# Performance work log

Measured on AMD Instinct MI355X. Metric: run time of the kernel, lower is better.

## Reference

```python
import jax, jax.numpy as jnp
import numpy as np

T, H, I, E, TOPK = 4096, 2880, 2880, 16, 4
EPS = 1e-5
ALPHA = 1.702


def setup_inputs() -> dict:
    key = jax.random.key(0)
    ks = jax.random.split(key, 8)
    s = 0.02
    return {
        "x": jax.random.normal(ks[0], (T, H), dtype=jnp.float32),
        "norm_w": jnp.ones((H,), dtype=jnp.float32),
        "gate_w": jax.random.normal(ks[1], (E, H), dtype=jnp.float32) * s,
        "gate_b": jax.random.normal(ks[2], (E,), dtype=jnp.float32) * s,
        "w1": jax.random.normal(ks[3], (E, 2 * I, H), dtype=jnp.float32) * s,  # fused gate_up
        "b1": jax.random.normal(ks[4], (E, 2 * I), dtype=jnp.float32) * s,
        "w2": jax.random.normal(ks[5], (E, H, I), dtype=jnp.float32) * s,      # down proj
        "b2": jax.random.normal(ks[6], (E, H), dtype=jnp.float32) * s,
    }


def _rmsnorm(x, w, eps=EPS):
    var = jnp.mean(x * x, axis=-1, keepdims=True)
    return x * jax.lax.rsqrt(var + eps) * w


def _swiglu(gu):
    glu, lin = jnp.split(gu, 2, axis=-1)
    return glu * jax.nn.sigmoid(ALPHA * glu) * (lin + 1.0)


def reference(x, norm_w, gate_w, gate_b, w1, b1, w2, b2):
    t = _rmsnorm(x, norm_w)                       # [T, H]
    logits = t @ gate_w.T + gate_b                # [T, E]
    # Renormalize routing: top-k of logits, softmax over the k selected logits
    vals, idx = jax.lax.top_k(logits, TOPK)       # [T, k]
    wts = jax.nn.softmax(vals, axis=-1)           # [T, k]
    combine = jnp.zeros((t.shape[0], E), dtype=t.dtype)
    combine = combine.at[jnp.arange(t.shape[0])[:, None], idx].set(wts)  # [T, E]
    out = jnp.zeros_like(x)
    for e in range(E):                            # small fixed expert loop
        gu = t @ w1[e].T + b1[e]                  # [T, 2I]
        y = _swiglu(gu) @ w2[e].T + b2[e]         # [T, H]
        out = out + combine[:, e:e + 1] * y
    return x + out
```

## Files before the change

### kernel.cpp

```cpp
#include <hip/hip_runtime.h>
#include <hip/hip_bf16.h>
#include <math.h>
#include <stdint.h>

#define T_TOK 4096
#define H_DIM 2880
#define E_NUM 16
#define ALPHA 1.702f
#define EPS_RMS 1e-5f

#define PADM 192
#define BK 32
#define NK (H_DIM / BK)
#define MAX_RT 104
#define NCT1 30
#define NCT2 15
#define G1 (MAX_RT * NCT1)
#define G2 (MAX_RT * NCT2)
#define ABUF 12288
#define BBUF 12288
#define BOFF 36864

typedef __attribute__((ext_vector_type(8))) short short8;
typedef __attribute__((ext_vector_type(4))) float f32x4;

__device__ __forceinline__ unsigned short f2bf(float f) {
  unsigned u = __float_as_uint(f);
  return (unsigned short)((u + 0x7fffu + ((u >> 16) & 1u)) >> 16);
}
__device__ __forceinline__ unsigned cpk(float a, float b) {
  unsigned r;
  asm("v_cvt_pk_bf16_f32 %0, %1, %2" : "=v"(r) : "v"(a), "v"(b));
  return r;
}
__device__ __forceinline__ float bf2f(unsigned short s) {
  return __uint_as_float((unsigned)s << 16);
}
__device__ __forceinline__ void gl_lds16(const void* g, unsigned char* lds_dst) {
  __builtin_amdgcn_global_load_lds(
      (const __attribute__((address_space(1))) void*)g,
      (__attribute__((address_space(3))) void*)lds_dst, 16, 0, 0);
}
#define ENDSTEP() do {                                           \
    asm volatile("s_waitcnt lgkmcnt(0)" ::: "memory");           \
    __builtin_amdgcn_s_barrier();                                \
    __builtin_amdgcn_sched_barrier(0);                           \
  } while (0)

__global__ __launch_bounds__(256) void k_norm_gate(
    const float* __restrict__ x, const float* __restrict__ norm_w,
    const float* __restrict__ gate_w, const float* __restrict__ gate_b,
    unsigned short* __restrict__ t_out,
    int* __restrict__ topk_id, float* __restrict__ topk_w,
    int* __restrict__ counts)
{
  int t = blockIdx.x, tid = threadIdx.x;
  const float4* xr = (const float4*)(x + (size_t)t * H_DIM);
  float4 xa[3];
  float ss = 0.f;
  int j = 0;
  for (int i = tid; i < 720; i += 256, j++) {
    float4 v = xr[i]; xa[j] = v;
    ss += v.x * v.x + v.y * v.y + v.z * v.z + v.w * v.w;
  }
#pragma unroll
  for (int o = 1; o < 64; o <<= 1) ss += __shfl_xor(ss, o, 64);
  __shared__ float red[4];
  if ((tid & 63) == 0) red[tid >> 6] = ss;
  __syncthreads();
  float rs = rsqrtf((red[0] + red[1] + red[2] + red[3]) * (1.f / H_DIM) + EPS_RMS);

  float part[16];
#pragma unroll
  for (int q = 0; q < 16; q++) part[q] = 0.f;
  j = 0;
  for (int i = tid; i < 720; i += 256, j++) {
    float4 v = xa[j];
    float4 w = ((const float4*)norm_w)[i];
    float t0 = v.x * rs * w.x, t1 = v.y * rs * w.y;
    float t2 = v.z * rs * w.z, t3 = v.w * rs * w.w;
    ushort4 b; b.x = f2bf(t0); b.y = f2bf(t1); b.z = f2bf(t2); b.w = f2bf(t3);
    ((ushort4*)(t_out + (size_t)t * H_DIM))[i] = b;
#pragma unroll
    for (int q = 0; q < 16; q++) {
      float4 g = ((const float4*)(gate_w + (size_t)q * H_DIM))[i];
      part[q] += t0 * g.x + t1 * g.y + t2 * g.z + t3 * g.w;
    }
  }
  __shared__ float lg[4][16];
#pragma unroll
  for (int q = 0; q < 16; q++) {
    float p = part[q];
#pragma unroll
    for (int o = 1; o < 64; o <<= 1) p += __shfl_xor(p, o, 64);
    if ((tid & 63) == 0) lg[tid >> 6][q] = p;
  }
  __syncthreads();
  if (tid == 0) {
    float logit[16];
    for (int q = 0; q < 16; q++)
      logit[q] = lg[0][q] + lg[1][q] + lg[2][q] + lg[3][q] + gate_b[q];
    unsigned used = 0; int idx[4]; float val[4];
    for (int k = 0; k < 4; k++) {
      float best = -3.4e38f; int bi = 0;
      for (int q = 0; q < 16; q++)
        if (!((used >> q) & 1u) && logit[q] > best) { best = logit[q]; bi = q; }
      used |= 1u << bi; idx[k] = bi; val[k] = best;
    }
    float s0 = 0.f, w4[4];
    for (int k = 0; k < 4; k++) { w4[k] = expf(val[k] - val[0]); s0 += w4[k]; }
    for (int k = 0; k < 4; k++) {
      topk_id[t * 4 + k] = idx[k];
      topk_w[t * 4 + k] = w4[k] / s0;
      atomicAdd(&counts[idx[k]], 1);
    }
  }
}

__global__ void k_offsets(const int* __restrict__ counts, int* __restrict__ d_off) {
  if (threadIdx.x == 0) {
    int acc = 0;
    for (int q = 0; q < 16; q++) {
      d_off[q] = acc;
      acc += ((counts[q] + PADM - 1) / PADM) * PADM;
    }
    d_off[16] = acc;
  }
}

__global__ __launch_bounds__(256) void k_fill(
    const int* __restrict__ topk_id, const float* __restrict__ topk_w,
    const int* __restrict__ counts, const int* __restrict__ d_off,
    int* __restrict__ perm_tok, float* __restrict__ perm_w,
    int* __restrict__ perm_sl)
{
  int e = blockIdx.x;
  int base = d_off[e], pe = d_off[e + 1] - base, cnt = counts[e];
  int tid = threadIdx.x, lane = tid & 63, wv = tid >> 6;
  __shared__ int wsum[4];
  int pos = 0;
  for (int c0 = 0; c0 < T_TOK; c0 += 256) {
    int tok = c0 + tid;
    int4 ids = ((const int4*)topk_id)[tok];
    int flag = 0, slot = 0;
    if (ids.x == e) { flag = 1; slot = 0; }
    else if (ids.y == e) { flag = 1; slot = 1; }
    else if (ids.z == e) { flag = 1; slot = 2; }
    else if (ids.w == e) { flag = 1; slot = 3; }
    unsigned long long b = __ballot(flag);
    int wprefix = __popcll(b & ((1ULL << lane) - 1ULL));
    if (lane == 0) wsum[wv] = __popcll(b);
    __syncthreads();
    int woff = 0;
    for (int i = 0; i < wv; i++) woff += wsum[i];
    int tot = wsum[0] + wsum[1] + wsum[2] + wsum[3];
    if (flag) {
      int p = base + pos + woff + wprefix;
      perm_tok[p] = tok;
      perm_w[p] = topk_w[tok * 4 + slot];
      perm_sl[p] = slot;
    }
    pos += tot;
    __syncthreads();
  }
  for (int i = cnt + tid; i < pe; i += 256) {
    perm_tok[base + i] = -1;
    perm_w[base + i] = 0.f;
    perm_sl[base + i] = 0;
  }
}

#define STAGE_A(abuf, ktn) do {                                               \
  _Pragma("unroll")                                                           \
  for (int i = 0; i < 3; i++)                                                 \
    gl_lds16(aptr[i] + (size_t)(ktn) * BK, lds + (abuf) * ABUF + adst[i]);    \
} while (0)

#define LOAD_B(ktn) do {                                                      \
  _Pragma("unroll")                                                           \
  for (int j = 0; j < 3; j++) {                                               \
    bv[j][0] = bptr[j][(ktn) * 8];                                            \
    bv[j][1] = bptr[j][(ktn) * 8 + 1];                                        \
  }                                                                           \
} while (0)

#define PACK_B(bbuf) do {                                                     \
  _Pragma("unroll")                                                           \
  for (int j = 0; j < 3; j++) {                                               \
    uint4 p;                                                                  \
    p.x = cpk(bv[j][0].x, bv[j][0].y); p.y = cpk(bv[j][0].z, bv[j][0].w);     \
    p.z = cpk(bv[j][1].x, bv[j][1].y); p.w = cpk(bv[j][1].z, bv[j][1].w);     \
    *(uint4*)(lds + BOFF + (bbuf) * BBUF + bdst[j]) = p;                      \
  }                                                                           \
} while (0)

#define COMPUTE(abuf, bbuf) do {                                              \
  const unsigned char* Abase = lds + (abuf) * ABUF + abase_off;               \
  const unsigned char* Bbase = lds + BOFF + (bbuf) * BBUF + bbase_off;        \
  short8 a0 = *(const short8*)(Abase);                                        \
  short8 a1 = *(const short8*)(Abase + 1024);                                 \
  short8 a2 = *(const short8*)(Abase + 2048);                                 \
  __builtin_amdgcn_s_setprio(1);                                              \
  _Pragma("unroll")                                                           \
  for (int n = 0; n < 12; n++) {                                              \
    short8 b = *(const short8*)(Bbase + n * 1024);                            \
    acc[0][n] = __builtin_amdgcn_mfma_f32_16x16x32_bf16(a0, b, acc[0][n], 0, 0, 0); \
    acc[1][n] = __builtin_amdgcn_mfma_f32_16x16x32_bf16(a1, b, acc[1][n], 0, 0, 0); \
    acc[2][n] = __builtin_amdgcn_mfma_f32_16x16x32_bf16(a2, b, acc[2][n], 0, 0, 0); \
  }                                                                           \
  __builtin_amdgcn_s_setprio(0);                                              \
} while (0)

#define GEMM_PIPE() do {                                                      \
  STAGE_A(0, 0); STAGE_A(1, 1); LOAD_B(0);                                    \
  PACK_B(0);                                                                  \
  ENDSTEP();                                                                  \
  int ca = 0;                                                                 \
  _Pragma("unroll 1")                                                         \
  for (int u = 0; u < NK / 2; u++) {                                          \
    int kt = 2 * u;                                                           \
    int ca1 = ca + 1; if (ca1 >= 3) ca1 -= 3;                                 \
    int ca2 = ca + 2; if (ca2 >= 3) ca2 -= 3;                                 \
    if (kt + 1 < NK) LOAD_B(kt + 1);                                          \
    if (kt + 2 < NK) STAGE_A(ca2, kt + 2);                                    \
    COMPUTE(ca, 0);                                                           \
    if (kt + 1 < NK) PACK_B(1);                                               \
    ENDSTEP();                                                                \
    if (kt + 2 < NK) LOAD_B(kt + 2);                                          \
    if (kt + 3 < NK) STAGE_A(ca, kt + 3);                                     \
    COMPUTE(ca1, 1);                                                          \
    if (kt + 2 < NK) PACK_B(0);                                               \
    ENDSTEP();                                                                \
    ca = ca2;                                                                 \
  }                                                                           \
} while (0)

__global__ __launch_bounds__(256, 2) void k_gemm1(
    const unsigned short* __restrict__ t_bf16,
    const float* __restrict__ w1, const float* __restrict__ b1,
    const int* __restrict__ perm_tok, const int* __restrict__ d_off,
    unsigned short* __restrict__ act)
{
  __shared__ __align__(16) unsigned char lds[3 * ABUF + 2 * BBUF];
  const int total = d_off[16];
  int bid = blockIdx.x;
  int wg = (bid & 7) * (G1 / 8) + (bid >> 3);
  int ct = wg / MAX_RT, rt = wg % MAX_RT;
  int rowbase = rt * PADM;
  if (rowbase >= total) return;
  int e = 0;
#pragma unroll
  for (int q = 0; q < E_NUM; q++) if (d_off[q + 1] <= rowbase) e = q + 1;

  int tid = threadIdx.x, lane = tid & 63, wv = tid >> 6;
  int lr = lane & 15, ch = lane >> 4;
  unsigned swz16 = (unsigned)((ch ^ ((lr >> 1) & 3)) << 4);
  unsigned abase_off = (unsigned)(wv * 3072 + lr * 64) + swz16;
  unsigned bbase_off = (unsigned)(lr * 64) + swz16;

  const unsigned short* aptr[3]; unsigned adst[3];
#pragma unroll
  for (int i = 0; i < 3; i++) {
    int cl = tid + 256 * i;
    int r = cl >> 2, c = cl & 3;
    int tok = perm_tok[rowbase + r];
    if (tok < 0) tok = 0;
    aptr[i] = t_bf16 + (size_t)tok * H_DIM + ((c ^ ((r >> 1) & 3)) * 8);
    adst[i] = (unsigned)cl * 16;
  }
  const float4* bptr[3]; unsigned bdst[3];
#pragma unroll
  for (int j = 0; j < 3; j++) {
    int idx = tid + 256 * j;
    int rr = idx >> 2, c = idx & 3;
    size_t grow = (size_t)e * (2 * H_DIM) +
                  (rr < 96 ? (size_t)(ct * 96 + rr) : (size_t)(H_DIM + ct * 96 + (rr - 96)));
    bptr[j] = (const float4*)(w1 + grow * H_DIM) + c * 2;
    bdst[j] = (unsigned)(rr * 64 + ((c ^ ((rr >> 1) & 3)) << 4));
  }

  f32x4 zero = {0.f, 0.f, 0.f, 0.f};
  f32x4 acc[3][12];
#pragma unroll
  for (int m = 0; m < 3; m++)
#pragma unroll
    for (int n = 0; n < 12; n++) acc[m][n] = zero;
  float4 bv[3][2];

  GEMM_PIPE();

  int rq = lane >> 4;
#pragma unroll
  for (int m = 0; m < 3; m++) {
    int row0 = rowbase + wv * 48 + m * 16 + rq * 4;
#pragma unroll
    for (int n = 0; n < 6; n++) {
      int col = ct * 96 + n * 16 + lr;
      float bg = b1[(size_t)e * (2 * H_DIM) + col];
      float bl = b1[(size_t)e * (2 * H_DIM) + H_DIM + col];
#pragma unroll
      for (int j = 0; j < 4; j++) {
        float g = acc[m][n][j] + bg;
        float l = acc[m][n + 6][j] + bl;
        float s = 1.f / (1.f + __expf(-ALPHA * g));
        act[(size_t)(row0 + j) * H_DIM + col] = f2bf(g * s * (l + 1.f));
      }
    }
  }
}

__global__ __launch_bounds__(256, 2) void k_gemm2(
    const unsigned short* __restrict__ act,
    const float* __restrict__ w2, const float* __restrict__ b2,
    const int* __restrict__ perm_tok, const float* __restrict__ perm_w,
    const int* __restrict__ perm_sl, const int* __restrict__ d_off,
    unsigned short* __restrict__ yslot)
{
  __shared__ __align__(16) unsigned char lds[3 * ABUF + 2 * BBUF];
  __shared__ int stok[PADM]; __shared__ float swt[PADM]; __shared__ int ssl[PADM];
  const int total = d_off[16];
  int bid = blockIdx.x;
  int wg = (bid & 7) * (G2 / 8) + (bid >> 3);
  int ct = wg / MAX_RT, rt = wg % MAX_RT;
  int rowbase = rt * PADM;
  if (rowbase >= total) return;
  int e = 0;
#pragma unroll
  for (int q = 0; q < E_NUM; q++) if (d_off[q + 1] <= rowbase) e = q + 1;

  int tid = threadIdx.x, lane = tid & 63, wv = tid >> 6;
  int lr = lane & 15, ch = lane >> 4;
  unsigned swz16 = (unsigned)((ch ^ ((lr >> 1) & 3)) << 4);
  unsigned abase_off = (unsigned)(wv * 3072 + lr * 64) + swz16;
  unsigned bbase_off = (unsigned)(lr * 64) + swz16;

  if (tid < PADM) {
    stok[tid] = perm_tok[rowbase + tid];
    swt[tid] = perm_w[rowbase + tid];
    ssl[tid] = perm_sl[rowbase + tid];
  }

  const unsigned short* aptr[3]; unsigned adst[3];
#pragma unroll
  for (int i = 0; i < 3; i++) {
    int cl = tid + 256 * i;
    int r = cl >> 2, c = cl & 3;
    aptr[i] = act + (size_t)(rowbase + r) * H_DIM + ((c ^ ((r >> 1) & 3)) * 8);
    adst[i] = (unsigned)cl * 16;
  }
  const float4* bptr[3]; unsigned bdst[3];
#pragma unroll
  for (int j = 0; j < 3; j++) {
    int idx = tid + 256 * j;
    int rr = idx >> 2, c = idx & 3;
    size_t grow = (size_t)e * H_DIM + (size_t)(ct * 192 + rr);
    bptr[j] = (const float4*)(w2 + grow * H_DIM) + c * 2;
    bdst[j] = (unsigned)(rr * 64 + ((c ^ ((rr >> 1) & 3)) << 4));
  }

  f32x4 zero = {0.f, 0.f, 0.f, 0.f};
  f32x4 acc[3][12];
#pragma unroll
  for (int m = 0; m < 3; m++)
#pragma unroll
    for (int n = 0; n < 12; n++) acc[m][n] = zero;
  float4 bv[3][2];

  GEMM_PIPE();

  int rq = lane >> 4;
#pragma unroll
  for (int m = 0; m < 3; m++) {
    int rl0 = wv * 48 + m * 16 + rq * 4;
#pragma unroll
    for (int n = 0; n < 12; n++) {
      int col = ct * 192 + n * 16 + lr;
      float b2v = b2[(size_t)e * H_DIM + col];
#pragma unroll
      for (int j = 0; j < 4; j++) {
        int rl = rl0 + j;
        int tk = stok[rl];
        if (tk >= 0) {
          float y = (acc[m][n][j] + b2v) * swt[rl];
          yslot[((size_t)ssl[rl] * T_TOK + tk) * H_DIM + col] = f2bf(y);
        }
      }
    }
  }
}

__global__ __launch_bounds__(256) void k_comb(
    const float* __restrict__ x, const unsigned short* __restrict__ yslot,
    float* __restrict__ out)
{
  const int n8 = T_TOK * H_DIM / 8;
  int i = blockIdx.x * 256 + threadIdx.x;
  int stride = gridDim.x * 256;
  for (; i < n8; i += stride) {
    float4 x0 = ((const float4*)x)[2 * i];
    float4 x1 = ((const float4*)x)[2 * i + 1];
    float s[8] = {x0.x, x0.y, x0.z, x0.w, x1.x, x1.y, x1.z, x1.w};
#pragma unroll
    for (int k = 0; k < 4; k++) {
      uint4 v = ((const uint4*)(yslot + (size_t)k * T_TOK * H_DIM))[i];
      unsigned u[4] = {v.x, v.y, v.z, v.w};
#pragma unroll
      for (int q = 0; q < 4; q++) {
        s[2 * q]     += __uint_as_float(u[q] << 16);
        s[2 * q + 1] += __uint_as_float(u[q] & 0xffff0000u);
      }
    }
    float4 o0 = {s[0], s[1], s[2], s[3]};
    float4 o1 = {s[4], s[5], s[6], s[7]};
    ((float4*)out)[2 * i] = o0;
    ((float4*)out)[2 * i + 1] = o1;
  }
}

extern "C" void kernel_launch(void* const* d_in, const int* in_sizes, int n_in,
                              void* d_out, int out_size, void* d_ws, size_t ws_size,
                              hipStream_t stream)
{
  const float* x      = (const float*)d_in[0];
  const float* norm_w = (const float*)d_in[1];
  const float* gate_w = (const float*)d_in[2];
  const float* gate_b = (const float*)d_in[3];
  const float* w1     = (const float*)d_in[4];
  const float* b1     = (const float*)d_in[5];
  const float* w2     = (const float*)d_in[6];
  const float* b2     = (const float*)d_in[7];
  float* out = (float*)d_out;
  char* ws = (char*)d_ws;

  unsigned short* t_bf16  = (unsigned short*)(ws);
  unsigned short* act     = (unsigned short*)(ws + 23592960);
  int*            topk_id = (int*)(ws + 138608640);
  float*          topk_w  = (float*)(ws + 138674176);
  int*            perm_tk = (int*)(ws + 138739712);
  float*          perm_w  = (float*)(ws + 138819584);
  int*            perm_sl = (int*)(ws + 138899456);
  int*            counts  = (int*)(ws + 138979328);
  int*            d_off   = (int*)(ws + 138979392);
  unsigned short* yslot   = (unsigned short*)(ws + 138979840);

  hipMemsetAsync(counts, 0, 64, stream);
  hipLaunchKernelGGL(k_norm_gate, dim3(T_TOK), dim3(256), 0, stream,
                     x, norm_w, gate_w, gate_b, t_bf16, topk_id, topk_w, counts);
  hipLaunchKernelGGL(k_offsets, dim3(1), dim3(64), 0, stream, counts, d_off);
  hipLaunchKernelGGL(k_fill, dim3(16), dim3(256), 0, stream,
                     topk_id, topk_w, counts, d_off, perm_tk, perm_w, perm_sl);
  hipLaunchKernelGGL(k_gemm1, dim3(G1), dim3(256), 0, stream,
                     t_bf16, w1, b1, perm_tk, d_off, act);
  hipLaunchKernelGGL(k_gemm2, dim3(G2), dim3(256), 0, stream,
                     act, w2, b2, perm_tk, perm_w, perm_sl, d_off, yslot);
  hipLaunchKernelGGL(k_comb, dim3(2048), dim3(256), 0, stream, x, yslot, out);
}
```

Measured before the change: 1.489 ms.

## Warp-specialize MoE GEMMs with a dedicated producer wave and smaller row tile

Both expert GEMM kernels now split each 256-thread block into one producer wave and three consumer waves. The producer stages A through global-to-LDS loads and converts fp32 weights to bf16 into double-buffered LDS, while the consumers only run MFMAs, synchronized by block barriers. The row tile shrinks from 192 to 144 rows (3 waves x 48) to match, which reduces padding waste but raises the tile count and the number of weight re-reads per row. The single producer wave now carries all the load and pack work, and per-wave register pressure for its two 12x2 float4 sets is high.

Result: slower. 2.234 ms (+50.0%).

```diff
diff --git a/kernel.cpp b/kernel.cpp
--- a/kernel.cpp
+++ b/kernel.cpp
@@ -9,17 +9,17 @@
 #define ALPHA 1.702f
 #define EPS_RMS 1e-5f
 
-#define PADM 192
+#define PADM 144
 #define BK 32
 #define NK (H_DIM / BK)
-#define MAX_RT 104
+#define MAX_RT 136
 #define NCT1 30
 #define NCT2 15
 #define G1 (MAX_RT * NCT1)
 #define G2 (MAX_RT * NCT2)
-#define ABUF 12288
+#define ABUF 9216
 #define BBUF 12288
-#define BOFF 36864
+#define BBOFF 27648
 
 typedef __attribute__((ext_vector_type(8))) short short8;
 typedef __attribute__((ext_vector_type(4))) float f32x4;
@@ -32,9 +32,6 @@
   unsigned r;
   asm("v_cvt_pk_bf16_f32 %0, %1, %2" : "=v"(r) : "v"(a), "v"(b));
   return r;
-}
-__device__ __forceinline__ float bf2f(unsigned short s) {
-  return __uint_as_float((unsigned)s << 16);
 }
 __device__ __forceinline__ void gl_lds16(const void* g, unsigned char* lds_dst) {
   __builtin_amdgcn_global_load_lds(
@@ -170,33 +167,72 @@
   }
 }
 
-#define STAGE_A(abuf, ktn) do {                                               \
+#define P_STAGE_A(abuf, ktn) do {                                             \
   _Pragma("unroll")                                                           \
-  for (int i = 0; i < 3; i++)                                                 \
-    gl_lds16(aptr[i] + (size_t)(ktn) * BK, lds + (abuf) * ABUF + adst[i]);    \
-} while (0)
-
-#define LOAD_B(ktn) do {                                                      \
+  for (int i = 0; i < 9; i++)                                                 \
+    gl_lds16(aptr9[i] + (size_t)(ktn) * BK,                                   \
+             lds + (abuf) * ABUF + lofs + i * 1024);                          \
+} while (0)
+
+#define P_LOAD_B(set, ktn) do {                                               \
   _Pragma("unroll")                                                           \
-  for (int j = 0; j < 3; j++) {                                               \
-    bv[j][0] = bptr[j][(ktn) * 8];                                            \
-    bv[j][1] = bptr[j][(ktn) * 8 + 1];                                        \
-  }                                                                           \
-} while (0)
-
-#define PACK_B(bbuf) do {                                                     \
+  for (int j = 0; j < 6; j++) {                                               \
+    set[j][0] = pg4[j * 11520 + (ktn) * 8 + c4 * 2];                          \
+    set[j][1] = pg4[j * 11520 + (ktn) * 8 + c4 * 2 + 1];                      \
+  }                                                                           \
   _Pragma("unroll")                                                           \
-  for (int j = 0; j < 3; j++) {                                               \
+  for (int j = 0; j < 6; j++) {                                               \
+    set[j + 6][0] = pl4[j * 11520 + (ktn) * 8 + c4 * 2];                      \
+    set[j + 6][1] = pl4[j * 11520 + (ktn) * 8 + c4 * 2 + 1];                  \
+  }                                                                           \
+} while (0)
+
+#define P_PACK_B(set, bbuf) do {                                              \
+  _Pragma("unroll")                                                           \
+  for (int j = 0; j < 12; j++) {                                              \
     uint4 p;                                                                  \
-    p.x = cpk(bv[j][0].x, bv[j][0].y); p.y = cpk(bv[j][0].z, bv[j][0].w);     \
-    p.z = cpk(bv[j][1].x, bv[j][1].y); p.w = cpk(bv[j][1].z, bv[j][1].w);     \
-    *(uint4*)(lds + BOFF + (bbuf) * BBUF + bdst[j]) = p;                      \
-  }                                                                           \
-} while (0)
-
-#define COMPUTE(abuf, bbuf) do {                                              \
-  const unsigned char* Abase = lds + (abuf) * ABUF + abase_off;               \
-  const unsigned char* Bbase = lds + BOFF + (bbuf) * BBUF + bbase_off;        \
+    p.x = cpk(set[j][0].x, set[j][0].y); p.y = cpk(set[j][0].z, set[j][0].w); \
+    p.z = cpk(set[j][1].x, set[j][1].y); p.w = cpk(set[j][1].z, set[j][1].w); \
+    *(uint4*)(lds + BBOFF + (bbuf) * BBUF + pwoff + j * 1024) = p;            \
+  }                                                                           \
+} while (0)
+
+#define PSTEP(AS, ktn2, LD, PK, PB) do {                                      \
+  P_STAGE_A(AS, ktn2);                                                        \
+  P_LOAD_B(LD, ktn2);                                                         \
+  __builtin_amdgcn_sched_barrier(0);                                          \
+  P_PACK_B(PK, PB);                                                           \
+  ENDSTEP();                                                                  \
+} while (0)
+
+#define PRODUCER_PIPE() do {                                                  \
+  P_STAGE_A(0, 0); P_STAGE_A(1, 1);                                           \
+  P_LOAD_B(bvA, 0);                                                           \
+  __builtin_amdgcn_sched_barrier(0);                                          \
+  P_PACK_B(bvA, 0);                                                           \
+  P_LOAD_B(bvB, 1);                                                           \
+  ENDSTEP();                                                                  \
+  _Pragma("unroll 1")                                                         \
+  for (int u = 0; u < 14; u++) {                                              \
+    int kt = 6 * u;                                                           \
+    PSTEP(2, kt + 2, bvA, bvB, 1);                                            \
+    PSTEP(0, kt + 3, bvB, bvA, 0);                                            \
+    PSTEP(1, kt + 4, bvA, bvB, 1);                                            \
+    PSTEP(2, kt + 5, bvB, bvA, 0);                                            \
+    PSTEP(0, kt + 6, bvA, bvB, 1);                                            \
+    PSTEP(1, kt + 7, bvB, bvA, 0);                                            \
+  }                                                                           \
+  PSTEP(2, 86, bvA, bvB, 1);                                       \
+  PSTEP(0, 87, bvB, bvA, 0);                                       \
+  PSTEP(1, 88, bvA, bvB, 1);                                       \
+  PSTEP(2, 89, bvB, bvA, 0);                                       \
+  P_PACK_B(bvB, 1); ENDSTEP();                         \
+  ENDSTEP();                                                       \
+} while (0)
+
+#define COMPUTE(ab, bb) do {                                                  \
+  const unsigned char* Abase = lds + (ab) * ABUF + abase_off;                 \
+  const unsigned char* Bbase = lds + BBOFF + (bb) * BBUF + bbase_off;         \
   short8 a0 = *(const short8*)(Abase);                                        \
   short8 a1 = *(const short8*)(Abase + 1024);                                 \
   short8 a2 = *(const short8*)(Abase + 2048);                                 \
@@ -211,27 +247,14 @@
   __builtin_amdgcn_s_setprio(0);                                              \
 } while (0)
 
-#define GEMM_PIPE() do {                                                      \
-  STAGE_A(0, 0); STAGE_A(1, 1); LOAD_B(0);                                    \
-  PACK_B(0);                                                                  \
-  ENDSTEP();                                                                  \
-  int ca = 0;                                                                 \
+#define CSTEP(ab, bb) do { COMPUTE(ab, bb); ENDSTEP(); } while (0)
+
+#define CONSUMER_PIPE() do {                                                  \
+  ENDSTEP();                           \
   _Pragma("unroll 1")                                                         \
-  for (int u = 0; u < NK / 2; u++) {                                          \
-    int kt = 2 * u;                                                           \
-    int ca1 = ca + 1; if (ca1 >= 3) ca1 -= 3;                                 \
-    int ca2 = ca + 2; if (ca2 >= 3) ca2 -= 3;                                 \
-    if (kt + 1 < NK) LOAD_B(kt + 1);                                          \
-    if (kt + 2 < NK) STAGE_A(ca2, kt + 2);                                    \
-    COMPUTE(ca, 0);                                                           \
-    if (kt + 1 < NK) PACK_B(1);                                               \
-    ENDSTEP();                                                                \
-    if (kt + 2 < NK) LOAD_B(kt + 2);                                          \
-    if (kt + 3 < NK) STAGE_A(ca, kt + 3);                                     \
-    COMPUTE(ca1, 1);                                                          \
-    if (kt + 2 < NK) PACK_B(0);                                               \
-    ENDSTEP();                                                                \
-    ca = ca2;                                                                 \
+  for (int u = 0; u < 15; u++) {                                              \
+    CSTEP(0, 0); CSTEP(1, 1); CSTEP(2, 0);                                    \
+    CSTEP(0, 1); CSTEP(1, 0); CSTEP(2, 1);                                    \
   }                                                                           \
 } while (0)
 
@@ -253,57 +276,54 @@
   for (int q = 0; q < E_NUM; q++) if (d_off[q + 1] <= rowbase) e = q + 1;
 
   int tid = threadIdx.x, lane = tid & 63, wv = tid >> 6;
-  int lr = lane & 15, ch = lane >> 4;
-  unsigned swz16 = (unsigned)((ch ^ ((lr >> 1) & 3)) << 4);
-  unsigned abase_off = (unsigned)(wv * 3072 + lr * 64) + swz16;
-  unsigned bbase_off = (unsigned)(lr * 64) + swz16;
-
-  const unsigned short* aptr[3]; unsigned adst[3];
-#pragma unroll
-  for (int i = 0; i < 3; i++) {
-    int cl = tid + 256 * i;
-    int r = cl >> 2, c = cl & 3;
-    int tok = perm_tok[rowbase + r];
-    if (tok < 0) tok = 0;
-    aptr[i] = t_bf16 + (size_t)tok * H_DIM + ((c ^ ((r >> 1) & 3)) * 8);
-    adst[i] = (unsigned)cl * 16;
-  }
-  const float4* bptr[3]; unsigned bdst[3];
-#pragma unroll
-  for (int j = 0; j < 3; j++) {
-    int idx = tid + 256 * j;
-    int rr = idx >> 2, c = idx & 3;
-    size_t grow = (size_t)e * (2 * H_DIM) +
-                  (rr < 96 ? (size_t)(ct * 96 + rr) : (size_t)(H_DIM + ct * 96 + (rr - 96)));
-    bptr[j] = (const float4*)(w1 + grow * H_DIM) + c * 2;
-    bdst[j] = (unsigned)(rr * 64 + ((c ^ ((rr >> 1) & 3)) << 4));
-  }
-
-  f32x4 zero = {0.f, 0.f, 0.f, 0.f};
-  f32x4 acc[3][12];
-#pragma unroll
-  for (int m = 0; m < 3; m++)
-#pragma unroll
-    for (int n = 0; n < 12; n++) acc[m][n] = zero;
-  float4 bv[3][2];
-
-  GEMM_PIPE();
-
-  int rq = lane >> 4;
-#pragma unroll
-  for (int m = 0; m < 3; m++) {
-    int row0 = rowbase + wv * 48 + m * 16 + rq * 4;
-#pragma unroll
-    for (int n = 0; n < 6; n++) {
-      int col = ct * 96 + n * 16 + lr;
-      float bg = b1[(size_t)e * (2 * H_DIM) + col];
-      float bl = b1[(size_t)e * (2 * H_DIM) + H_DIM + col];
-#pragma unroll
-      for (int j = 0; j < 4; j++) {
-        float g = acc[m][n][j] + bg;
-        float l = acc[m][n + 6][j] + bl;
-        float s = 1.f / (1.f + __expf(-ALPHA * g));
-        act[(size_t)(row0 + j) * H_DIM + col] = f2bf(g * s * (l + 1.f));
+
+  if (wv == 3) {
+    int r0 = lane >> 2, c4 = lane & 3;
+    int acs = (lane & 3) ^ ((lane >> 3) & 3);
+    unsigned lofs = (unsigned)lane * 16;
+    const unsigned short* aptr9[9];
+#pragma unroll
+    for (int i = 0; i < 9; i++) {
+      int tok = perm_tok[rowbase + r0 + 16 * i];
+      if (tok < 0) tok = 0;
+      aptr9[i] = t_bf16 + (size_t)tok * H_DIM + acs * 8;
+    }
+    size_t g0 = (size_t)e * (2 * H_DIM) + (size_t)(ct * 96) + r0;
+    const float4* pg4 = (const float4*)(w1 + g0 * H_DIM);
+    const float4* pl4 = (const float4*)(w1 + (g0 + H_DIM) * H_DIM);
+    unsigned pwoff = (unsigned)(r0 * 64) + ((unsigned)(c4 ^ ((r0 >> 1) & 3)) << 4);
+    float4 bvA[12][2], bvB[12][2];
+    PRODUCER_PIPE();
+  } else {
+    int lr = lane & 15, ch = lane >> 4;
+    unsigned swz16 = (unsigned)((ch ^ ((lr >> 1) & 3)) << 4);
+    unsigned abase_off = (unsigned)(wv * 3072 + lr * 64) + swz16;
+    unsigned bbase_off = (unsigned)(lr * 64) + swz16;
+    f32x4 zero = {0.f, 0.f, 0.f, 0.f};
+    f32x4 acc[3][12];
+#pragma unroll
+    for (int m = 0; m < 3; m++)
+#pragma unroll
+      for (int n = 0; n < 12; n++) acc[m][n] = zero;
+
+    CONSUMER_PIPE();
+
+    int rq = lane >> 4;
+#pragma unroll
+    for (int m = 0; m < 3; m++) {
+      int row0 = rowbase + wv * 48 + m * 16 + rq * 4;
+#pragma unroll
+      for (int n = 0; n < 6; n++) {
+        int col = ct * 96 + n * 16 + lr;
+        float bg = b1[(size_t)e * (2 * H_DIM) + col];
+        float bl = b1[(size_t)e * (2 * H_DIM) + H_DIM + col];
+#pragma unroll
+        for (int j = 0; j < 4; j++) {
+          float g = acc[m][n][j] + bg;
+          float l = acc[m][n + 6][j] + bl;
+          float s = 1.f / (1.f + __expf(-ALPHA * g));
+          act[(size_t)(row0 + j) * H_DIM + col] = f2bf(g * s * (l + 1.f));
+        }
       }
     }
   }
@@ -317,7 +337,6 @@
     unsigned short* __restrict__ yslot)
 {
   __shared__ __align__(16) unsigned char lds[3 * ABUF + 2 * BBUF];
-  __shared__ int stok[PADM]; __shared__ float swt[PADM]; __shared__ int ssl[PADM];
   const int total = d_off[16];
   int bid = blockIdx.x;
   int wg = (bid & 7) * (G2 / 8) + (bid >> 3);
@@ -329,60 +348,52 @@
   for (int q = 0; q < E_NUM; q++) if (d_off[q + 1] <= rowbase) e = q + 1;
 
   int tid = threadIdx.x, lane = tid & 63, wv = tid >> 6;
-  int lr = lane & 15, ch = lane >> 4;
-  unsigned swz16 = (unsigned)((ch ^ ((lr >> 1) & 3)) << 4);
-  unsigned abase_off = (unsigned)(wv * 3072 + lr * 64) + swz16;
-  unsigned bbase_off = (unsigned)(lr * 64) + swz16;
-
-  if (tid < PADM) {
-    stok[tid] = perm_tok[rowbase + tid];
-    swt[tid] = perm_w[rowbase + tid];
-    ssl[tid] = perm_sl[rowbase + tid];
-  }
-
-  const unsigned short* aptr[3]; unsigned adst[3];
-#pragma unroll
-  for (int i = 0; i < 3; i++) {
-    int cl = tid + 256 * i;
-    int r = cl >> 2, c = cl & 3;
-    aptr[i] = act + (size_t)(rowbase + r) * H_DIM + ((c ^ ((r >> 1) & 3)) * 8);
-    adst[i] = (unsigned)cl * 16;
-  }
-  const float4* bptr[3]; unsigned bdst[3];
-#pragma unroll
-  for (int j = 0; j < 3; j++) {
-    int idx = tid + 256 * j;
-    int rr = idx >> 2, c = idx & 3;
-    size_t grow = (size_t)e * H_DIM + (size_t)(ct * 192 + rr);
-    bptr[j] = (const float4*)(w2 + grow * H_DIM) + c * 2;
-    bdst[j] = (unsigned)(rr * 64 + ((c ^ ((rr >> 1) & 3)) << 4));
-  }
-
-  f32x4 zero = {0.f, 0.f, 0.f, 0.f};
-  f32x4 acc[3][12];
-#pragma unroll
-  for (int m = 0; m < 3; m++)
-#pragma unroll
-    for (int n = 0; n < 12; n++) acc[m][n] = zero;
-  float4 bv[3][2];
-
-  GEMM_PIPE();
-
-  int rq = lane >> 4;
-#pragma unroll
-  for (int m = 0; m < 3; m++) {
-    int rl0 = wv * 48 + m * 16 + rq * 4;
-#pragma unroll
-    for (int n = 0; n < 12; n++) {
-      int col = ct * 192 + n * 16 + lr;
-      float b2v = b2[(size_t)e * H_DIM + col];
+
+  if (wv == 3) {
+    int r0 = lane >> 2, c4 = lane & 3;
+    int acs = (lane & 3) ^ ((lane >> 3) & 3);
+    unsigned lofs = (unsigned)lane * 16;
+    const unsigned short* aptr9[9];
+#pragma unroll
+    for (int i = 0; i < 9; i++)
+      aptr9[i] = act + (size_t)(rowbase + r0 + 16 * i) * H_DIM + acs * 8;
+    size_t g0 = (size_t)e * H_DIM + (size_t)(ct * 192) + r0;
+    const float4* pg4 = (const float4*)(w2 + g0 * H_DIM);
+    const float4* pl4 = (const float4*)(w2 + (g0 + 96) * H_DIM);
+    unsigned pwoff = (unsigned)(r0 * 64) + ((unsigned)(c4 ^ ((r0 >> 1) & 3)) << 4);
+    float4 bvA[12][2], bvB[12][2];
+    PRODUCER_PIPE();
+  } else {
+    int lr = lane & 15, ch = lane >> 4;
+    unsigned swz16 = (unsigned)((ch ^ ((lr >> 1) & 3)) << 4);
+    unsigned abase_off = (unsigned)(wv * 3072 + lr * 64) + swz16;
+    unsigned bbase_off = (unsigned)(lr * 64) + swz16;
+    f32x4 zero = {0.f, 0.f, 0.f, 0.f};
+    f32x4 acc[3][12];
+#pragma unroll
+    for (int m = 0; m < 3; m++)
+#pragma unroll
+      for (int n = 0; n < 12; n++) acc[m][n] = zero;
+
+    CONSUMER_PIPE();
+
+    int rq = lane >> 4;
+#pragma unroll
+    for (int m = 0; m < 3; m++) {
+      int rl0 = wv * 48 + m * 16 + rq * 4;
 #pragma unroll
       for (int j = 0; j < 4; j++) {
         int rl = rl0 + j;
-        int tk = stok[rl];
+        int tk = perm_tok[rowbase + rl];
+        float w = perm_w[rowbase + rl];
+        int sl = perm_sl[rowbase + rl];
         if (tk >= 0) {
-          float y = (acc[m][n][j] + b2v) * swt[rl];
-          yslot[((size_t)ssl[rl] * T_TOK + tk) * H_DIM + col] = f2bf(y);
+#pragma unroll
+          for (int n = 0; n < 12; n++) {
+            int col = ct * 192 + n * 16 + lr;
+            float y = (acc[m][n][j] + b2[(size_t)e * H_DIM + col]) * w;
+            yslot[((size_t)sl * T_TOK + tk) * H_DIM + col] = f2bf(y);
+          }
         }
       }
     }
```

## Split expert GEMM tiles across eight waves with 4x2 wave layout

Applied to the files above, without the earlier changes.

Both expert GEMM kernels now run with 512-thread workgroups (8 waves) on the same 192x192 output tile. The waves form a 4x2 grid, so each wave holds half as many accumulators, and the global-to-LDS staging work is split between full and partial thread sets. The goal is more waves per CU to hide memory and LDS latency, and lower per-wave register pressure. The cost is more LDS fragment reads per MFMA. A launch-bounds hint of 4 blocks of 512 threads may cap registers tightly enough to force spills, and LDS use per block likely stops that occupancy being reached anyway.

After: 1.484 ms (median of 2 runs). Within noise of the previous version (-0.4%).

```diff
diff --git a/kernel.cpp b/kernel.cpp
--- a/kernel.cpp
+++ b/kernel.cpp
@@ -32,9 +32,6 @@
   unsigned r;
   asm("v_cvt_pk_bf16_f32 %0, %1, %2" : "=v"(r) : "v"(a), "v"(b));
   return r;
-}
-__device__ __forceinline__ float bf2f(unsigned short s) {
-  return __uint_as_float((unsigned)s << 16);
 }
 __device__ __forceinline__ void gl_lds16(const void* g, unsigned char* lds_dst) {
   __builtin_amdgcn_global_load_lds(
@@ -171,47 +168,30 @@
 }
 
 #define STAGE_A(abuf, ktn) do {                                               \
-  _Pragma("unroll")                                                           \
-  for (int i = 0; i < 3; i++)                                                 \
-    gl_lds16(aptr[i] + (size_t)(ktn) * BK, lds + (abuf) * ABUF + adst[i]);    \
+  gl_lds16(aptr0 + (size_t)(ktn) * BK, lds + (abuf) * ABUF + adst0);          \
+  if (tid < 256)                                                              \
+    gl_lds16(aptr1 + (size_t)(ktn) * BK, lds + (abuf) * ABUF + adst1);        \
 } while (0)
 
 #define LOAD_B(ktn) do {                                                      \
-  _Pragma("unroll")                                                           \
-  for (int j = 0; j < 3; j++) {                                               \
-    bv[j][0] = bptr[j][(ktn) * 8];                                            \
-    bv[j][1] = bptr[j][(ktn) * 8 + 1];                                        \
+  bv[0][0] = bptr0[(ktn) * 8]; bv[0][1] = bptr0[(ktn) * 8 + 1];               \
+  if (tid < 256) { bv[1][0] = bptr1[(ktn) * 8]; bv[1][1] = bptr1[(ktn) * 8 + 1]; } \
+} while (0)
+
+#define PACK_B(bbuf) do {                                                     \
+  uint4 p0;                                                                   \
+  p0.x = cpk(bv[0][0].x, bv[0][0].y); p0.y = cpk(bv[0][0].z, bv[0][0].w);     \
+  p0.z = cpk(bv[0][1].x, bv[0][1].y); p0.w = cpk(bv[0][1].z, bv[0][1].w);     \
+  *(uint4*)(lds + BOFF + (bbuf) * BBUF + bdst0) = p0;                         \
+  if (tid < 256) {                                                            \
+    uint4 p1;                                                                 \
+    p1.x = cpk(bv[1][0].x, bv[1][0].y); p1.y = cpk(bv[1][0].z, bv[1][0].w);   \
+    p1.z = cpk(bv[1][1].x, bv[1][1].y); p1.w = cpk(bv[1][1].z, bv[1][1].w);   \
+    *(uint4*)(lds + BOFF + (bbuf) * BBUF + bdst1) = p1;                       \
   }                                                                           \
 } while (0)
 
-#define PACK_B(bbuf) do {                                                     \
-  _Pragma("unroll")                                                           \
-  for (int j = 0; j < 3; j++) {                                               \
-    uint4 p;                                                                  \
-    p.x = cpk(bv[j][0].x, bv[j][0].y); p.y = cpk(bv[j][0].z, bv[j][0].w);     \
-    p.z = cpk(bv[j][1].x, bv[j][1].y); p.w = cpk(bv[j][1].z, bv[j][1].w);     \
-    *(uint4*)(lds + BOFF + (bbuf) * BBUF + bdst[j]) = p;                      \
-  }                                                                           \
-} while (0)
-
-#define COMPUTE(abuf, bbuf) do {                                              \
-  const unsigned char* Abase = lds + (abuf) * ABUF + abase_off;               \
-  const unsigned char* Bbase = lds + BOFF + (bbuf) * BBUF + bbase_off;        \
-  short8 a0 = *(const short8*)(Abase);                                        \
-  short8 a1 = *(const short8*)(Abase + 1024);                                 \
-  short8 a2 = *(const short8*)(Abase + 2048);                                 \
-  __builtin_amdgcn_s_setprio(1);                                              \
-  _Pragma("unroll")                                                           \
-  for (int n = 0; n < 12; n++) {                                              \
-    short8 b = *(const short8*)(Bbase + n * 1024);                            \
-    acc[0][n] = __builtin_amdgcn_mfma_f32_16x16x32_bf16(a0, b, acc[0][n], 0, 0, 0); \
-    acc[1][n] = __builtin_amdgcn_mfma_f32_16x16x32_bf16(a1, b, acc[1][n], 0, 0, 0); \
-    acc[2][n] = __builtin_amdgcn_mfma_f32_16x16x32_bf16(a2, b, acc[2][n], 0, 0, 0); \
-  }                                                                           \
-  __builtin_amdgcn_s_setprio(0);                                              \
-} while (0)
-
-#define GEMM_PIPE() do {                                                      \
+#define GEMM_PIPE(COMP) do {                                                  \
   STAGE_A(0, 0); STAGE_A(1, 1); LOAD_B(0);                                    \
   PACK_B(0);                                                                  \
   ENDSTEP();                                                                  \
@@ -223,19 +203,57 @@
     int ca2 = ca + 2; if (ca2 >= 3) ca2 -= 3;                                 \
     if (kt + 1 < NK) LOAD_B(kt + 1);                                          \
     if (kt + 2 < NK) STAGE_A(ca2, kt + 2);                                    \
-    COMPUTE(ca, 0);                                                           \
+    COMP(ca, 0);                                                              \
     if (kt + 1 < NK) PACK_B(1);                                               \
     ENDSTEP();                                                                \
     if (kt + 2 < NK) LOAD_B(kt + 2);                                          \
     if (kt + 3 < NK) STAGE_A(ca, kt + 3);                                     \
-    COMPUTE(ca1, 1);                                                          \
+    COMP(ca1, 1);                                                             \
     if (kt + 2 < NK) PACK_B(0);                                               \
     ENDSTEP();                                                                \
     ca = ca2;                                                                 \
   }                                                                           \
 } while (0)
 
-__global__ __launch_bounds__(256, 2) void k_gemm1(
+#define COMP1(ab, bb) do {                                                    \
+  const unsigned char* Ab = lds + (ab) * ABUF;                                \
+  const unsigned char* Bb = lds + BOFF + (bb) * BBUF;                         \
+  short8 a0 = *(const short8*)(Ab + abase);                                   \
+  short8 a1 = *(const short8*)(Ab + abase + 1024);                            \
+  short8 a2 = *(const short8*)(Ab + abase + 2048);                            \
+  __builtin_amdgcn_s_setprio(1);                                              \
+  _Pragma("unroll")                                                           \
+  for (int n = 0; n < 3; n++) {                                               \
+    short8 bg = *(const short8*)(Bb + bgbase + n * 1024);                     \
+    short8 bl = *(const short8*)(Bb + blbase + n * 1024);                     \
+    accg[0][n] = __builtin_amdgcn_mfma_f32_16x16x32_bf16(a0, bg, accg[0][n], 0, 0, 0); \
+    accg[1][n] = __builtin_amdgcn_mfma_f32_16x16x32_bf16(a1, bg, accg[1][n], 0, 0, 0); \
+    accg[2][n] = __builtin_amdgcn_mfma_f32_16x16x32_bf16(a2, bg, accg[2][n], 0, 0, 0); \
+    accl[0][n] = __builtin_amdgcn_mfma_f32_16x16x32_bf16(a0, bl, accl[0][n], 0, 0, 0); \
+    accl[1][n] = __builtin_amdgcn_mfma_f32_16x16x32_bf16(a1, bl, accl[1][n], 0, 0, 0); \
+    accl[2][n] = __builtin_amdgcn_mfma_f32_16x16x32_bf16(a2, bl, accl[2][n], 0, 0, 0); \
+  }                                                                           \
+  __builtin_amdgcn_s_setprio(0);                                              \
+} while (0)
+
+#define COMP2(ab, bb) do {                                                    \
+  const unsigned char* Ab = lds + (ab) * ABUF;                                \
+  const unsigned char* Bb = lds + BOFF + (bb) * BBUF;                         \
+  short8 a0 = *(const short8*)(Ab + abase);                                   \
+  short8 a1 = *(const short8*)(Ab + abase + 1024);                            \
+  short8 a2 = *(const short8*)(Ab + abase + 2048);                            \
+  __builtin_amdgcn_s_setprio(1);                                              \
+  _Pragma("unroll")                                                           \
+  for (int n = 0; n < 6; n++) {                                               \
+    short8 b = *(const short8*)(Bb + bbase + n * 1024);                       \
+    acc[0][n] = __builtin_amdgcn_mfma_f32_16x16x32_bf16(a0, b, acc[0][n], 0, 0, 0); \
+    acc[1][n] = __builtin_amdgcn_mfma_f32_16x16x32_bf16(a1, b, acc[1][n], 0, 0, 0); \
+    acc[2][n] = __builtin_amdgcn_mfma_f32_16x16x32_bf16(a2, b, acc[2][n], 0, 0, 0); \
+  }                                                                           \
+  __builtin_amdgcn_s_setprio(0);                                              \
+} while (0)
+
+__global__ __launch_bounds__(512, 4) void k_gemm1(
     const unsigned short* __restrict__ t_bf16,
     const float* __restrict__ w1, const float* __restrict__ b1,
     const int* __restrict__ perm_tok, const int* __restrict__ d_off,
@@ -253,55 +271,66 @@
   for (int q = 0; q < E_NUM; q++) if (d_off[q + 1] <= rowbase) e = q + 1;
 
   int tid = threadIdx.x, lane = tid & 63, wv = tid >> 6;
+  int wm = wv & 3, wn = wv >> 2;
   int lr = lane & 15, ch = lane >> 4;
   unsigned swz16 = (unsigned)((ch ^ ((lr >> 1) & 3)) << 4);
-  unsigned abase_off = (unsigned)(wv * 3072 + lr * 64) + swz16;
-  unsigned bbase_off = (unsigned)(lr * 64) + swz16;
-
-  const unsigned short* aptr[3]; unsigned adst[3];
-#pragma unroll
-  for (int i = 0; i < 3; i++) {
-    int cl = tid + 256 * i;
-    int r = cl >> 2, c = cl & 3;
-    int tok = perm_tok[rowbase + r];
-    if (tok < 0) tok = 0;
-    aptr[i] = t_bf16 + (size_t)tok * H_DIM + ((c ^ ((r >> 1) & 3)) * 8);
-    adst[i] = (unsigned)cl * 16;
-  }
-  const float4* bptr[3]; unsigned bdst[3];
-#pragma unroll
-  for (int j = 0; j < 3; j++) {
-    int idx = tid + 256 * j;
-    int rr = idx >> 2, c = idx & 3;
+  unsigned abase  = (unsigned)((wm * 48 + lr) * 64) + swz16;
+  unsigned bgbase = (unsigned)((wn * 48 + lr) * 64) + swz16;
+  unsigned blbase = bgbase + 6144;
+
+  const unsigned short* aptr0; const unsigned short* aptr1 = 0;
+  unsigned adst0, adst1 = 0;
+  {
+    int cl = tid, r = cl >> 2, c = cl & 3;
+    int tok = perm_tok[rowbase + r]; if (tok < 0) tok = 0;
+    aptr0 = t_bf16 + (size_t)tok * H_DIM + ((c ^ ((r >> 1) & 3)) * 8);
+    adst0 = (unsigned)cl * 16;
+  }
+  if (tid < 256) {
+    int cl = 512 + tid, r = cl >> 2, c = cl & 3;
+    int tok = perm_tok[rowbase + r]; if (tok < 0) tok = 0;
+    aptr1 = t_bf16 + (size_t)tok * H_DIM + ((c ^ ((r >> 1) & 3)) * 8);
+    adst1 = (unsigned)cl * 16;
+  }
+  const float4* bptr0; const float4* bptr1 = 0;
+  unsigned bdst0, bdst1 = 0;
+  {
+    int cl = tid, rr = cl >> 2, c = cl & 3;
     size_t grow = (size_t)e * (2 * H_DIM) +
                   (rr < 96 ? (size_t)(ct * 96 + rr) : (size_t)(H_DIM + ct * 96 + (rr - 96)));
-    bptr[j] = (const float4*)(w1 + grow * H_DIM) + c * 2;
-    bdst[j] = (unsigned)(rr * 64 + ((c ^ ((rr >> 1) & 3)) << 4));
+    bptr0 = (const float4*)(w1 + grow * H_DIM) + c * 2;
+    bdst0 = (unsigned)(rr * 64 + ((c ^ ((rr >> 1) & 3)) << 4));
+  }
+  if (tid < 256) {
+    int cl = 512 + tid, rr = cl >> 2, c = cl & 3;
+    size_t grow = (size_t)(H_DIM + ct * 96 + (rr - 96)) + (size_t)e * (2 * H_DIM);
+    bptr1 = (const float4*)(w1 + grow * H_DIM) + c * 2;
+    bdst1 = (unsigned)(rr * 64 + ((c ^ ((rr >> 1) & 3)) << 4));
   }
 
   f32x4 zero = {0.f, 0.f, 0.f, 0.f};
-  f32x4 acc[3][12];
+  f32x4 accg[3][3], accl[3][3];
 #pragma unroll
   for (int m = 0; m < 3; m++)
 #pragma unroll
-    for (int n = 0; n < 12; n++) acc[m][n] = zero;
-  float4 bv[3][2];
-
-  GEMM_PIPE();
+    for (int n = 0; n < 3; n++) { accg[m][n] = zero; accl[m][n] = zero; }
+  float4 bv[2][2];
+
+  GEMM_PIPE(COMP1);
 
   int rq = lane >> 4;
 #pragma unroll
   for (int m = 0; m < 3; m++) {
-    int row0 = rowbase + wv * 48 + m * 16 + rq * 4;
-#pragma unroll
-    for (int n = 0; n < 6; n++) {
-      int col = ct * 96 + n * 16 + lr;
+    int row0 = rowbase + wm * 48 + m * 16 + rq * 4;
+#pragma unroll
+    for (int n = 0; n < 3; n++) {
+      int col = ct * 96 + wn * 48 + n * 16 + lr;
       float bg = b1[(size_t)e * (2 * H_DIM) + col];
       float bl = b1[(size_t)e * (2 * H_DIM) + H_DIM + col];
 #pragma unroll
       for (int j = 0; j < 4; j++) {
-        float g = acc[m][n][j] + bg;
-        float l = acc[m][n + 6][j] + bl;
+        float g = accg[m][n][j] + bg;
+        float l = accl[m][n][j] + bl;
         float s = 1.f / (1.f + __expf(-ALPHA * g));
         act[(size_t)(row0 + j) * H_DIM + col] = f2bf(g * s * (l + 1.f));
       }
@@ -309,7 +338,7 @@
   }
 }
 
-__global__ __launch_bounds__(256, 2) void k_gemm2(
+__global__ __launch_bounds__(512, 4) void k_gemm2(
     const unsigned short* __restrict__ act,
     const float* __restrict__ w2, const float* __restrict__ b2,
     const int* __restrict__ perm_tok, const float* __restrict__ perm_w,
@@ -329,10 +358,11 @@
   for (int q = 0; q < E_NUM; q++) if (d_off[q + 1] <= rowbase) e = q + 1;
 
   int tid = threadIdx.x, lane = tid & 63, wv = tid >> 6;
+  int wm = wv & 3, wn = wv >> 2;
   int lr = lane & 15, ch = lane >> 4;
   unsigned swz16 = (unsigned)((ch ^ ((lr >> 1) & 3)) << 4);
-  unsigned abase_off = (unsigned)(wv * 3072 + lr * 64) + swz16;
-  unsigned bbase_off = (unsigned)(lr * 64) + swz16;
+  unsigned abase = (unsigned)((wm * 48 + lr) * 64) + swz16;
+  unsigned bbase = (unsigned)((wn * 96 + lr) * 64) + swz16;
 
   if (tid < PADM) {
     stok[tid] = perm_tok[rowbase + tid];
@@ -340,41 +370,50 @@
     ssl[tid] = perm_sl[rowbase + tid];
   }
 
-  const unsigned short* aptr[3]; unsigned adst[3];
-#pragma unroll
-  for (int i = 0; i < 3; i++) {
-    int cl = tid + 256 * i;
-    int r = cl >> 2, c = cl & 3;
-    aptr[i] = act + (size_t)(rowbase + r) * H_DIM + ((c ^ ((r >> 1) & 3)) * 8);
-    adst[i] = (unsigned)cl * 16;
-  }
-  const float4* bptr[3]; unsigned bdst[3];
-#pragma unroll
-  for (int j = 0; j < 3; j++) {
-    int idx = tid + 256 * j;
-    int rr = idx >> 2, c = idx & 3;
+  const unsigned short* aptr0; const unsigned short* aptr1 = 0;
+  unsigned adst0, adst1 = 0;
+  {
+    int cl = tid, r = cl >> 2, c = cl & 3;
+    aptr0 = act + (size_t)(rowbase + r) * H_DIM + ((c ^ ((r >> 1) & 3)) * 8);
+    adst0 = (unsigned)cl * 16;
+  }
+  if (tid < 256) {
+    int cl = 512 + tid, r = cl >> 2, c = cl & 3;
+    aptr1 = act + (size_t)(rowbase + r) * H_DIM + ((c ^ ((r >> 1) & 3)) * 8);
+    adst1 = (unsigned)cl * 16;
+  }
+  const float4* bptr0; const float4* bptr1 = 0;
+  unsigned bdst0, bdst1 = 0;
+  {
+    int cl = tid, rr = cl >> 2, c = cl & 3;
     size_t grow = (size_t)e * H_DIM + (size_t)(ct * 192 + rr);
-    bptr[j] = (const float4*)(w2 + grow * H_DIM) + c * 2;
-    bdst[j] = (unsigned)(rr * 64 + ((c ^ ((rr >> 1) & 3)) << 4));
+    bptr0 = (const float4*)(w2 + grow * H_DIM) + c * 2;
+    bdst0 = (unsigned)(rr * 64 + ((c ^ ((rr >> 1) & 3)) << 4));
+  }
+  if (tid < 256) {
+    int cl = 512 + tid, rr = cl >> 2, c = cl & 3;
+    size_t grow = (size_t)e * H_DIM + (size_t)(ct * 192 + rr);
+    bptr1 = (const float4*)(w2 + grow * H_DIM) + c * 2;
+    bdst1 = (unsigned)(rr * 64 + ((c ^ ((rr >> 1) & 3)) << 4));
   }
 
   f32x4 zero = {0.f, 0.f, 0.f, 0.f};
-  f32x4 acc[3][12];
+  f32x4 acc[3][6];
 #pragma unroll
   for (int m = 0; m < 3; m++)
 #pragma unroll
-    for (int n = 0; n < 12; n++) acc[m][n] = zero;
-  float4 bv[3][2];
-
-  GEMM_PIPE();
+    for (int n = 0; n < 6; n++) acc[m][n] = zero;
+  float4 bv[2][2];
+
+  GEMM_PIPE(COMP2);
 
   int rq = lane >> 4;
 #pragma unroll
   for (int m = 0; m < 3; m++) {
-    int rl0 = wv * 48 + m * 16 + rq * 4;
-#pragma unroll
-    for (int n = 0; n < 12; n++) {
-      int col = ct * 192 + n * 16 + lr;
+    int rl0 = wm * 48 + m * 16 + rq * 4;
+#pragma unroll
+    for (int n = 0; n < 6; n++) {
+      int col = ct * 192 + wn * 96 + n * 16 + lr;
       float b2v = b2[(size_t)e * H_DIM + col];
 #pragma unroll
       for (int j = 0; j < 4; j++) {
@@ -449,9 +488,9 @@
   hipLaunchKernelGGL(k_offsets, dim3(1), dim3(64), 0, stream, counts, d_off);
   hipLaunchKernelGGL(k_fill, dim3(16), dim3(256), 0, stream,
                      topk_id, topk_w, counts, d_off, perm_tk, perm_w, perm_sl);
-  hipLaunchKernelGGL(k_gemm1, dim3(G1), dim3(256), 0, stream,
+  hipLaunchKernelGGL(k_gemm1, dim3(G1), dim3(512), 0, stream,
                      t_bf16, w1, b1, perm_tk, d_off, act);
-  hipLaunchKernelGGL(k_gemm2, dim3(G2), dim3(256), 0, stream,
+  hipLaunchKernelGGL(k_gemm2, dim3(G2), dim3(512), 0, stream,
                      act, w2, b2, perm_tk, perm_w, perm_sl, d_off, yslot);
   hipLaunchKernelGGL(k_comb, dim3(2048), dim3(256), 0, stream, x, yslot, out);
 }
```
